# Optimization experiments

Measured on AMD Instinct MI355X. Metric: run time of the kernel, lower is better.

Reference implementation:

```python
import jax, jax.numpy as jnp
import numpy as np

B, T, C = 2, 2048, 2048
H, G, HS = 16, 4, 128       # n_head, n_query_groups, head_size
N_ELEM = 128                # rotary_percentage * head_size
D_FF = 4 * C
EPS = 1e-5


def layer_norm(x, w, b):
    mu = jnp.mean(x, axis=-1, keepdims=True)
    var = jnp.var(x, axis=-1, keepdims=True)
    return (x - mu) * jax.lax.rsqrt(var + EPS) * w + b


def apply_rope(x, cos, sin):
    # x: (B, H, T, n_elem); cos/sin: (T, n_elem) with freqs duplicated over halves
    half = x.shape[-1] // 2
    x1, x2 = x[..., :half], x[..., half:]
    rotated = jnp.concatenate((-x2, x1), axis=-1)
    return x * cos + rotated * sin


def setup_inputs() -> dict:
    key = jax.random.key(0)
    ks = jax.random.split(key, 8)
    x = jax.random.normal(ks[0], (B, T, C), dtype=jnp.float32)
    # RoPE cache (neox/llama style, duplicated halves to match half-rotation apply_rope)
    inv_freq = 1.0 / (10000.0 ** (jnp.arange(0, N_ELEM, 2, dtype=jnp.float32) / N_ELEM))
    freqs = jnp.outer(jnp.arange(T, dtype=jnp.float32), inv_freq)  # (T, n_elem/2)
    cos = jnp.concatenate((jnp.cos(freqs), jnp.cos(freqs)), axis=-1)
    sin = jnp.concatenate((jnp.sin(freqs), jnp.sin(freqs)), axis=-1)
    mask = jnp.tril(jnp.ones((T, T), dtype=bool))
    s = 0.02
    qkv_w = jax.random.normal(ks[1], ((H + 2 * G) * HS, C), dtype=jnp.float32) * s
    proj_w = jax.random.normal(ks[2], (C, C), dtype=jnp.float32) * s
    fc1_w = jax.random.normal(ks[3], (D_FF, C), dtype=jnp.float32) * s
    fc2_w = jax.random.normal(ks[4], (C, D_FF), dtype=jnp.float32) * s
    return {
        "x": x, "cos": cos, "sin": sin, "mask": mask,
        "ln1_w": jnp.ones((C,), jnp.float32), "ln1_b": jnp.zeros((C,), jnp.float32),
        "qkv_w": qkv_w, "proj_w": proj_w,
        "ln2_w": jnp.ones((C,), jnp.float32), "ln2_b": jnp.zeros((C,), jnp.float32),
        "fc1_w": fc1_w, "fc1_b": jnp.zeros((D_FF,), jnp.float32),
        "fc2_w": fc2_w, "fc2_b": jnp.zeros((C,), jnp.float32),
    }


def block_forward(x, cos, sin, mask, ln1_w, ln1_b, qkv_w, proj_w,
                  ln2_w, ln2_b, fc1_w, fc1_b, fc2_w, fc2_b):
    q_per_kv = H // G
    # --- LayerNormLinear: LN then fused QKV projection ---
    qkv = layer_norm(x, ln1_w, ln1_b) @ qkv_w.T            # (B, T, (H+2G)*HS)
    qkv = qkv.reshape(B, T, G, q_per_kv + 2, HS).transpose(0, 2, 3, 1, 4)
    q = qkv[:, :, :q_per_kv]                               # (B, G, q_per_kv, T, HS)
    k = qkv[:, :, q_per_kv:q_per_kv + 1]                   # (B, G, 1, T, HS)
    v = qkv[:, :, q_per_kv + 1:]
    # GQA expansion (repeat_interleave over the per-group axis)
    k = jnp.repeat(k, q_per_kv, axis=2)
    v = jnp.repeat(v, q_per_kv, axis=2)
    q = q.reshape(B, H, T, HS)
    k = k.reshape(B, H, T, HS)
    v = v.reshape(B, H, T, HS)
    # --- RoPE on first N_ELEM channels ---
    q = jnp.concatenate((apply_rope(q[..., :N_ELEM], cos, sin), q[..., N_ELEM:]), axis=-1)
    k = jnp.concatenate((apply_rope(k[..., :N_ELEM], cos, sin), k[..., N_ELEM:]), axis=-1)
    # --- SDPA with boolean mask ---
    scale = 1.0 / jnp.sqrt(jnp.asarray(HS, q.dtype))
    att = jnp.einsum("bhqd,bhkd->bhqk", q, k) * scale
    att = jnp.where(mask, att, jnp.finfo(att.dtype).min)
    att = jax.nn.softmax(att, axis=-1)
    y = jnp.einsum("bhqk,bhkd->bhqd", att, v)
    y = y.transpose(0, 2, 1, 3).reshape(B, T, C)
    h = y @ proj_w.T
    # --- non-parallel residual: x += attn; x += MLP(LN(x)) ---
    x = x + h
    mlp = jax.nn.gelu(layer_norm(x, ln2_w, ln2_b) @ fc1_w.T + fc1_b, approximate=False)
    x = x + (mlp @ fc2_w.T + fc2_b)
    return x


def reference(x, cos, sin, mask, ln1_w, ln1_b, qkv_w, proj_w,
              ln2_w, ln2_b, fc1_w, fc1_b, fc2_w, fc2_b):
    return block_forward(x, cos, sin, mask, ln1_w, ln1_b, qkv_w, proj_w,
                         ln2_w, ln2_b, fc1_w, fc1_b, fc2_w, fc2_b)
```

## Files before the change

### kernel.cpp

```cpp
#include <hip/hip_runtime.h>

typedef __bf16 bf16;
typedef __bf16 bf16x8 __attribute__((ext_vector_type(8)));
typedef __bf16 bf16x4 __attribute__((ext_vector_type(4)));
typedef float  f32x4  __attribute__((ext_vector_type(4)));

#define LOG2E 1.4426950408889634f

__device__ __forceinline__ void gload_lds16(const void* g, void* l) {
    __builtin_amdgcn_global_load_lds(
        (__attribute__((address_space(1))) const void*)g,
        (__attribute__((address_space(3))) void*)l, 16, 0, 0);
}

__global__ __launch_bounds__(256) void cvt_bf16(const float* __restrict__ src,
                                                bf16* __restrict__ dst, int n) {
    int i = (blockIdx.x * 256 + threadIdx.x) * 4;
    if (i + 3 < n) {
        float4 v = *(const float4*)(src + i);
        bf16x4 o;
        o[0] = (bf16)v.x; o[1] = (bf16)v.y; o[2] = (bf16)v.z; o[3] = (bf16)v.w;
        *(bf16x4*)(dst + i) = o;
    }
}

__global__ __launch_bounds__(256) void ln_kernel(const float* __restrict__ x,
                                                 const float* __restrict__ wgt,
                                                 const float* __restrict__ bias,
                                                 bf16* __restrict__ out) {
    __shared__ float red[8];
    const int tid = threadIdx.x;
    const int lane = tid & 63, w = tid >> 6;
    const size_t row = blockIdx.x;
    const float4* xr = (const float4*)(x + row * 2048);
    float4 v0 = xr[tid];
    float4 v1 = xr[tid + 256];
    float s = v0.x + v0.y + v0.z + v0.w + v1.x + v1.y + v1.z + v1.w;
    float q = v0.x*v0.x + v0.y*v0.y + v0.z*v0.z + v0.w*v0.w
            + v1.x*v1.x + v1.y*v1.y + v1.z*v1.z + v1.w*v1.w;
    #pragma unroll
    for (int off = 32; off; off >>= 1) {
        s += __shfl_xor(s, off);
        q += __shfl_xor(q, off);
    }
    if (lane == 0) { red[w] = s; red[4 + w] = q; }
    __syncthreads();
    float S  = red[0] + red[1] + red[2] + red[3];
    float Q2 = red[4] + red[5] + red[6] + red[7];
    float mu = S * (1.0f / 2048.0f);
    float var = Q2 * (1.0f / 2048.0f) - mu * mu;
    float rstd = rsqrtf(var + 1e-5f);

    bf16* orow = out + row * 2048;
    int c0 = tid * 4;
    float vv[8] = {v0.x, v0.y, v0.z, v0.w, v1.x, v1.y, v1.z, v1.w};
    bf16x4 o;
    #pragma unroll
    for (int k = 0; k < 4; ++k)
        o[k] = (bf16)((vv[k] - mu) * rstd * wgt[c0 + k] + bias[c0 + k]);
    *(bf16x4*)(orow + c0) = o;
    #pragma unroll
    for (int k = 0; k < 4; ++k)
        o[k] = (bf16)((vv[4 + k] - mu) * rstd * wgt[1024 + c0 + k] + bias[1024 + c0 + k]);
    *(bf16x4*)(orow + 1024 + c0) = o;
}

template <int EPI>
__global__ __launch_bounds__(512, 4) void gemmB(const bf16* __restrict__ A,
                                                const bf16* __restrict__ B,
                                                void* __restrict__ OutP,
                                                const float* __restrict__ bias,
                                                const float* __restrict__ res,
                                                int M, int N, int K) {
    __shared__ __align__(16) char lds[65536];
    const int tid = threadIdx.x;
    const int lane = tid & 63;
    const int w = tid >> 6, wr = w >> 1, wc = w & 1;
    const int lo = lane & 15, hi = lane >> 4;

    const int nwg = gridDim.x;
    const int bid = blockIdx.x;
    const int q = nwg >> 3, r = nwg & 7, xcd = bid & 7, off = bid >> 3;
    const int s = (xcd < r ? xcd * (q + 1) : r * (q + 1) + (xcd - r) * q) + off;
    const int MB = M / 128;
    const int sq = s >> 6, wi = s & 63;
    const int nsqm = MB >> 3;
    const int gm = sq % nsqm, gn = sq / nsqm;
    const int brow = (gm * 8 + (wi & 7)) * 128;
    const int bcol = (gn * 8 + (wi >> 3)) * 128;

    const int sr = tid >> 3;
    const int su = (tid & 7) ^ (sr & 7);
    const bf16* Ag = A + (size_t)(brow + sr) * K + su * 8;
    const bf16* Bg = B + (size_t)(bcol + sr) * K + su * 8;
    const size_t K64 = (size_t)64 * K;
    char* dst0 = lds + tid * 16;

    auto stage = [&](int bf, int kt) {
        char* d = dst0 + bf * 32768;
        gload_lds16(Ag + kt * 64, d);
        gload_lds16(Ag + K64 + kt * 64, d + 8192);
        gload_lds16(Bg + kt * 64, d + 16384);
        gload_lds16(Bg + K64 + kt * 64, d + 24576);
    };

    f32x4 acc[2][4] = {};
    const int NT = K >> 6;

    stage(0, 0);
    for (int kt = 0; kt < NT; ++kt) {
        const int cur = kt & 1;
        if (kt + 1 < NT) {
            stage(cur ^ 1, kt + 1);
            asm volatile("s_waitcnt vmcnt(4)" ::: "memory");
        } else {
            asm volatile("s_waitcnt vmcnt(0)" ::: "memory");
        }
        __builtin_amdgcn_s_barrier();

        const char* ab = lds + cur * 32768;
        const char* bb = ab + 16384;
        bf16x8 af[2][2], bfv[4][2];
        #pragma unroll
        for (int m = 0; m < 2; ++m) {
            const int rA = wr * 32 + m * 16 + lo;
            #pragma unroll
            for (int ks = 0; ks < 2; ++ks)
                af[m][ks] = *(const bf16x8*)(ab + rA * 128 + (((ks * 4 + hi) ^ (lo & 7)) << 4));
        }
        #pragma unroll
        for (int n = 0; n < 4; ++n) {
            const int rB = wc * 64 + n * 16 + lo;
            #pragma unroll
            for (int ks = 0; ks < 2; ++ks)
                bfv[n][ks] = *(const bf16x8*)(bb + rB * 128 + (((ks * 4 + hi) ^ (lo & 7)) << 4));
        }
        __builtin_amdgcn_s_setprio(1);
        #pragma unroll
        for (int m = 0; m < 2; ++m)
            #pragma unroll
            for (int n = 0; n < 4; ++n)
                #pragma unroll
                for (int ks = 0; ks < 2; ++ks)
                    acc[m][n] = __builtin_amdgcn_mfma_f32_16x16x32_bf16(af[m][ks], bfv[n][ks], acc[m][n], 0, 0, 0);
        __builtin_amdgcn_s_setprio(0);
        __builtin_amdgcn_s_barrier();
    }

    float* outF = (float*)OutP;
    bf16*  outB = (bf16*)OutP;
    #pragma unroll
    for (int n = 0; n < 4; ++n) {
        const int col = bcol + wc * 64 + n * 16 + lo;
        float bv = 0.f;
        if (EPI == 1 || EPI == 3) bv = bias[col];
        #pragma unroll
        for (int m = 0; m < 2; ++m) {
            #pragma unroll
            for (int rr = 0; rr < 4; ++rr) {
                const int row = brow + wr * 32 + m * 16 + hi * 4 + rr;
                float v = acc[m][n][rr];
                if (EPI == 0) {
                    outB[(size_t)row * N + col] = (bf16)v;
                } else if (EPI == 1) {
                    v += bv;
                    v = 0.5f * v * (1.0f + erff(v * 0.70710678118654752f));
                    outB[(size_t)row * N + col] = (bf16)v;
                } else if (EPI == 2) {
                    outF[(size_t)row * N + col] = res[(size_t)row * N + col] + v;
                } else {
                    outF[(size_t)row * N + col] = res[(size_t)row * N + col] + v + bv;
                }
            }
        }
    }
}

__global__ __launch_bounds__(256) void rope_scatter(const bf16* __restrict__ qkv,
                                                    const float* __restrict__ cosb,
                                                    const float* __restrict__ sinb,
                                                    bf16* __restrict__ Q,
                                                    bf16* __restrict__ Kg) {
    const int tid = threadIdx.x;
    const int row = blockIdx.x;
    const int b = row >> 11, t = row & 2047;
    const bf16* src = qkv + (size_t)row * 3072;
    #pragma unroll
    for (int i = tid; i < 1280; i += 256) {
        int slot = i >> 6;
        int d = i & 63;
        int g = slot / 5, m = slot - g * 5;
        int msrc = g * 6 + m;
        float v1 = (float)src[msrc * 128 + d];
        float v2 = (float)src[msrc * 128 + d + 64];
        float c1 = cosb[t * 128 + d],      s1 = sinb[t * 128 + d];
        float c2 = cosb[t * 128 + d + 64], s2 = sinb[t * 128 + d + 64];
        float o1 = v1 * c1 - v2 * s1;
        float o2 = v2 * c2 + v1 * s2;
        if (m < 4) {
            int hh = g * 4 + m;
            size_t base = ((size_t)(b * 16 + hh) * 2048 + t) * 128;
            Q[base + d] = (bf16)o1;
            Q[base + d + 64] = (bf16)o2;
        } else {
            size_t base = ((size_t)(b * 4 + g) * 2048 + t) * 128;
            Kg[base + d] = (bf16)o1;
            Kg[base + d + 64] = (bf16)o2;
        }
    }
}

__global__ __launch_bounds__(256) void vtrans(const bf16* __restrict__ qkvo,
                                              bf16* __restrict__ Vt) {
    const int tid = threadIdx.x;
    const int t0 = blockIdx.x * 64;
    const int z  = blockIdx.y;
    const int b = z >> 2, g = z & 3;
    const int d = tid & 127;
    const int th = tid >> 7;
    const bf16* src = qkvo + (size_t)(b * 2048 + t0 + th * 32) * 3072 + g * 768 + 640 + d;
    bf16* dst = Vt + ((size_t)z * 128 + d) * 2048 + t0 + th * 32;
    #pragma unroll
    for (int c = 0; c < 4; ++c) {
        bf16x8 v;
        #pragma unroll
        for (int j = 0; j < 8; ++j)
            v[j] = src[(size_t)(c * 8 + j) * 3072];
        *(bf16x8*)(dst + c * 8) = v;
    }
}

__global__ __launch_bounds__(256) void attn_kernel(const bf16* __restrict__ Q,
                                                   const bf16* __restrict__ Kg,
                                                   const bf16* __restrict__ Vt,
                                                   bf16* __restrict__ Y) {
    __shared__ __align__(16) bf16 Ks[2][64 * 128];
    __shared__ __align__(16) bf16 Vs[2][128 * 64];
    __shared__ __align__(16) bf16 Ps[4][16 * 80];

    const int tid = threadIdx.x;
    const int lane = tid & 63, w = tid >> 6;
    const int lo = lane & 15, hi = lane >> 4;
    const int bh = blockIdx.y;
    const int b = bh >> 4, h = bh & 15;
    const int g = h >> 2;

    const bf16* Kbase = Kg + (size_t)(b * 4 + g) * 2048 * 128;
    const bf16* Vbase = Vt + (size_t)(b * 4 + g) * 128 * 2048;
    const float scale = 0.08838834764831845f;
    bf16* pw = &Ps[w][0];

    bf16x8 kreg[4], vreg[4];

    #pragma unroll 1
    for (int pass = 0; pass < 2; ++pass) {
        const int qt = pass ? 31 - (int)blockIdx.x : (int)blockIdx.x;
        const int q0 = qt * 64;

        bf16x8 qf[4];
        {
            const size_t qbase = ((size_t)bh * 2048 + q0 + w * 16 + lo) * 128;
            #pragma unroll
            for (int dd = 0; dd < 4; ++dd)
                qf[dd] = *(const bf16x8*)(Q + qbase + dd * 32 + hi * 8);
        }

        float m_r[4], l_r[4];
        f32x4 oacc[8] = {};
        #pragma unroll
        for (int rr = 0; rr < 4; ++rr) { m_r[rr] = -1e30f; l_r[rr] = 0.f; }

        #pragma unroll
        for (int it = 0; it < 4; ++it) {
            int ob = (it * 256 + tid) * 16;
            int rk = ob >> 8, cb = ob & 255;
            kreg[it] = *(const bf16x8*)(Kbase + (size_t)rk * 128 + (cb >> 1));
            int dv = ob >> 7, cv = ob & 127;
            vreg[it] = *(const bf16x8*)(Vbase + (size_t)dv * 2048 + (cv >> 1));
        }
        #pragma unroll
        for (int it = 0; it < 4; ++it) {
            int ob = (it * 256 + tid) * 16;
            int rk = ob >> 8, cb = ob & 255;
            *(bf16x8*)((char*)Ks[0] + rk * 256 + (cb ^ ((rk & 7) << 4))) = kreg[it];
            int dv = ob >> 7, cv = ob & 127;
            *(bf16x8*)((char*)Vs[0] + dv * 128 + (cv ^ ((dv & 7) << 4))) = vreg[it];
        }
        __syncthreads();
        int cur = 0;

        for (int kt = 0; kt <= qt; ++kt) {
            const bool pf = (kt < qt);
            if (pf) {
                #pragma unroll
                for (int it = 0; it < 4; ++it) {
                    int ob = (it * 256 + tid) * 16;
                    int rk = ob >> 8, cb = ob & 255;
                    kreg[it] = *(const bf16x8*)(Kbase + (size_t)((kt + 1) * 64 + rk) * 128 + (cb >> 1));
                    int dv = ob >> 7, cv = ob & 127;
                    vreg[it] = *(const bf16x8*)(Vbase + (size_t)dv * 2048 + (kt + 1) * 64 + (cv >> 1));
                }
            }

            const char* KsC = (const char*)Ks[cur];
            const char* VsC = (const char*)Vs[cur];

            f32x4 sj[4];
            __builtin_amdgcn_s_setprio(1);
            #pragma unroll
            for (int j = 0; j < 4; ++j) {
                f32x4 a = {};
                int rk = j * 16 + lo;
                #pragma unroll
                for (int dd = 0; dd < 4; ++dd) {
                    int cb = dd * 64 + hi * 16;
                    bf16x8 kf = *(const bf16x8*)(KsC + rk * 256 + (cb ^ ((rk & 7) << 4)));
                    a = __builtin_amdgcn_mfma_f32_16x16x32_bf16(qf[dd], kf, a, 0, 0, 0);
                }
                sj[j] = a;
            }
            __builtin_amdgcn_s_setprio(0);

            float sv[4][4];
            const bool diag = (kt == qt);
            #pragma unroll
            for (int j = 0; j < 4; ++j)
                #pragma unroll
                for (int rr = 0; rr < 4; ++rr) {
                    float v = sj[j][rr] * scale;
                    if (diag) {
                        int tg = kt * 64 + j * 16 + lo;
                        int qg = q0 + w * 16 + hi * 4 + rr;
                        if (tg > qg) v = -1e30f;
                    }
                    sv[j][rr] = v;
                }

            float mx[4];
            #pragma unroll
            for (int rr = 0; rr < 4; ++rr) {
                float m0 = fmaxf(fmaxf(sv[0][rr], sv[1][rr]), fmaxf(sv[2][rr], sv[3][rr]));
                #pragma unroll
                for (int off = 8; off; off >>= 1) m0 = fmaxf(m0, __shfl_xor(m0, off, 16));
                mx[rr] = m0;
            }

            bool need = false;
            #pragma unroll
            for (int rr = 0; rr < 4; ++rr) need = need || (mx[rr] > m_r[rr] + 8.0f);
            if (__any(need)) {
                #pragma unroll
                for (int rr = 0; rr < 4; ++rr) {
                    float mnew = fmaxf(m_r[rr], mx[rr]);
                    float al = exp2f((m_r[rr] - mnew) * LOG2E);
                    l_r[rr] *= al;
                    m_r[rr] = mnew;
                    #pragma unroll
                    for (int dn = 0; dn < 8; ++dn) oacc[dn][rr] *= al;
                }
            }

            float p[4][4];
            #pragma unroll
            for (int rr = 0; rr < 4; ++rr) {
                #pragma unroll
                for (int j = 0; j < 4; ++j)
                    p[j][rr] = exp2f((sv[j][rr] - m_r[rr]) * LOG2E);
                float s0 = p[0][rr] + p[1][rr] + p[2][rr] + p[3][rr];
                #pragma unroll
                for (int off = 8; off; off >>= 1) s0 += __shfl_xor(s0, off, 16);
                l_r[rr] += s0;
            }

            #pragma unroll
            for (int j = 0; j < 4; ++j)
                #pragma unroll
                for (int rr = 0; rr < 4; ++rr)
                    pw[(hi * 4 + rr) * 80 + j * 16 + lo] = (bf16)p[j][rr];

            __builtin_amdgcn_s_setprio(1);
            #pragma unroll
            for (int tc = 0; tc < 2; ++tc) {
                bf16x8 pf2 = *(const bf16x8*)(pw + lo * 80 + tc * 32 + hi * 8);
                #pragma unroll
                for (int dn = 0; dn < 8; ++dn) {
                    int rv = dn * 16 + lo;
                    int cv = tc * 64 + hi * 16;
                    bf16x8 vf = *(const bf16x8*)(VsC + rv * 128 + (cv ^ ((rv & 7) << 4)));
                    oacc[dn] = __builtin_amdgcn_mfma_f32_16x16x32_bf16(pf2, vf, oacc[dn], 0, 0, 0);
                }
            }
            __builtin_amdgcn_s_setprio(0);

            if (pf) {
                #pragma unroll
                for (int it = 0; it < 4; ++it) {
                    int ob = (it * 256 + tid) * 16;
                    int rk = ob >> 8, cb = ob & 255;
                    *(bf16x8*)((char*)Ks[cur ^ 1] + rk * 256 + (cb ^ ((rk & 7) << 4))) = kreg[it];
                    int dv = ob >> 7, cv = ob & 127;
                    *(bf16x8*)((char*)Vs[cur ^ 1] + dv * 128 + (cv ^ ((dv & 7) << 4))) = vreg[it];
                }
            }
            __syncthreads();
            cur ^= 1;
        }

        #pragma unroll
        for (int dn = 0; dn < 8; ++dn)
            #pragma unroll
            for (int rr = 0; rr < 4; ++rr) {
                int qg = q0 + w * 16 + hi * 4 + rr;
                Y[((size_t)b * 2048 + qg) * 2048 + h * 128 + dn * 16 + lo] =
                    (bf16)(oacc[dn][rr] / l_r[rr]);
            }
    }
}

extern "C" void kernel_launch(void* const* d_in, const int* in_sizes, int n_in,
                              void* d_out, int out_size, void* d_ws, size_t ws_size,
                              hipStream_t stream) {
    const float* x      = (const float*)d_in[0];
    const float* cosb   = (const float*)d_in[1];
    const float* sinb   = (const float*)d_in[2];
    const float* ln1_w  = (const float*)d_in[4];
    const float* ln1_b  = (const float*)d_in[5];
    const float* qkv_w  = (const float*)d_in[6];
    const float* proj_w = (const float*)d_in[7];
    const float* ln2_w  = (const float*)d_in[8];
    const float* ln2_b  = (const float*)d_in[9];
    const float* fc1_w  = (const float*)d_in[10];
    const float* fc1_b  = (const float*)d_in[11];
    const float* fc2_w  = (const float*)d_in[12];
    const float* fc2_b  = (const float*)d_in[13];
    float* out = (float*)d_out;

    char* ws = (char*)d_ws;
    bf16*  w_qkv  = (bf16*)(ws + 0ull);
    bf16*  w_proj = (bf16*)(ws + 12582912ull);
    bf16*  w_fc1  = (bf16*)(ws + 20971520ull);
    bf16*  w_fc2  = (bf16*)(ws + 54525952ull);
    float* x2     = (float*)(ws + 88080384ull);
    bf16*  lnout  = (bf16*)(ws + 121634816ull);
    char*  R      = ws + 138412032ull;
    bf16*  qkvo = (bf16*)(R);
    bf16*  Qb   = (bf16*)(R + 25165824ull);
    bf16*  Kb   = (bf16*)(R + 41943040ull);
    bf16*  Vtb  = (bf16*)(R + 46137344ull);
    bf16*  Yb   = (bf16*)(R + 50331648ull);
    bf16*  mlp  = (bf16*)(R);

    cvt_bf16<<<6144,  256, 0, stream>>>(qkv_w,  w_qkv,  3072 * 2048);
    cvt_bf16<<<4096,  256, 0, stream>>>(proj_w, w_proj, 2048 * 2048);
    cvt_bf16<<<16384, 256, 0, stream>>>(fc1_w,  w_fc1,  8192 * 2048);
    cvt_bf16<<<16384, 256, 0, stream>>>(fc2_w,  w_fc2,  2048 * 8192);

    ln_kernel<<<4096, 256, 0, stream>>>(x, ln1_w, ln1_b, lnout);

    gemmB<0><<<768, 512, 0, stream>>>(lnout, w_qkv, qkvo, nullptr, nullptr,
                                      4096, 3072, 2048);

    rope_scatter<<<4096, 256, 0, stream>>>(qkvo, cosb, sinb, Qb, Kb);
    vtrans<<<dim3(32, 8), 256, 0, stream>>>(qkvo, Vtb);

    attn_kernel<<<dim3(16, 32), 256, 0, stream>>>(Qb, Kb, Vtb, Yb);

    gemmB<2><<<512, 512, 0, stream>>>(Yb, w_proj, x2, nullptr, x,
                                      4096, 2048, 2048);

    ln_kernel<<<4096, 256, 0, stream>>>(x2, ln2_w, ln2_b, lnout);

    gemmB<1><<<2048, 512, 0, stream>>>(lnout, w_fc1, mlp, fc1_b, nullptr,
                                       4096, 8192, 2048);

    gemmB<3><<<512, 512, 0, stream>>>(mlp, w_fc2, out, fc2_b, x2,
                                      4096, 2048, 8192);
}
```

Before: 584.1 us.

## Use 256x256-tile GEMM with XCD-aware swizzle and split-K for MLP

Adds a new GEMM kernel with 256x256 output tiles per 512-thread block, double-buffered direct-to-LDS loads, XCD-aware block remapping with super-tile grouping, and setprio around MFMA bursts. It is used for fc1 (with fused GELU) and for fc2, which is split into two K halves. One half writes the residual-plus-bias result and the other writes a float partial, summed afterwards by an extra add kernel. The larger tiles aim to raise operand reuse and L2 locality, while split-K keeps enough blocks for fc2. The cost is an extra fp32 partial buffer round-trip and higher register pressure.

```diff
diff --git a/kernel.cpp b/kernel.cpp
--- a/kernel.cpp
+++ b/kernel.cpp
@@ -21,6 +21,17 @@
         bf16x4 o;
         o[0] = (bf16)v.x; o[1] = (bf16)v.y; o[2] = (bf16)v.z; o[3] = (bf16)v.w;
         *(bf16x4*)(dst + i) = o;
+    }
+}
+
+__global__ __launch_bounds__(256) void add_f32(float* __restrict__ out,
+                                               const float* __restrict__ p, int n) {
+    int i = (blockIdx.x * 256 + threadIdx.x) * 4;
+    if (i + 3 < n) {
+        float4 a = *(const float4*)(out + i);
+        float4 b = *(const float4*)(p + i);
+        a.x += b.x; a.y += b.y; a.z += b.z; a.w += b.w;
+        *(float4*)(out + i) = a;
     }
 }
 
@@ -170,6 +181,121 @@
                     outF[(size_t)row * N + col] = res[(size_t)row * N + col] + v;
                 } else {
                     outF[(size_t)row * N + col] = res[(size_t)row * N + col] + v + bv;
+                }
+            }
+        }
+    }
+}
+
+template <int EPI>
+__global__ __launch_bounds__(512, 2) void gemmE2(const bf16* __restrict__ A,
+                                                 const bf16* __restrict__ B,
+                                                 void* __restrict__ OutP,
+                                                 const float* __restrict__ bias,
+                                                 const float* __restrict__ res,
+                                                 float* __restrict__ Aux,
+                                                 int M, int N, int Kc, int ldk,
+                                                 int SQR, int SQC) {
+    extern __shared__ __align__(16) char lds[];
+    const int tid = threadIdx.x;
+    const int lane = tid & 63;
+    const int w = tid >> 6, wr = w >> 2, wc = w & 3;
+    const int lo = lane & 15, hi = lane >> 4;
+    const int koff = (EPI == 5) ? (int)blockIdx.y * Kc : 0;
+
+    const int nwg = gridDim.x;
+    const int bid = blockIdx.x;
+    const int q = nwg >> 3, r = nwg & 7, xcd = bid & 7, off = bid >> 3;
+    const int s = (xcd < r ? xcd * (q + 1) : r * (q + 1) + (xcd - r) * q) + off;
+    const int MB = M / 256;
+    const int sqsz = SQR * SQC;
+    const int sq = s / sqsz, wi = s % sqsz;
+    const int nsqm = MB / SQR;
+    const int gm = sq % nsqm, gn = sq / nsqm;
+    const int brow = (gm * SQR + wi % SQR) * 256;
+    const int bcol = (gn * SQC + wi / SQR) * 256;
+
+    const int srow = tid >> 2;
+    const int scol = ((tid & 3) ^ ((tid >> 3) & 3)) * 8;
+    const bf16* Ag = A + (size_t)(brow + srow) * ldk + koff + scol;
+    const bf16* Bg = B + (size_t)(bcol + srow) * ldk + koff + scol;
+    const size_t R128 = (size_t)128 * ldk;
+    char* d0 = lds + tid * 16;
+
+    auto stage = [&](int bf, int kt) {
+        char* d = d0 + bf * 32768;
+        gload_lds16(Ag + kt * 32, d);
+        gload_lds16(Ag + R128 + kt * 32, d + 8192);
+        gload_lds16(Bg + kt * 32, d + 16384);
+        gload_lds16(Bg + R128 + kt * 32, d + 24576);
+    };
+
+    f32x4 acc[8][4] = {};
+    const int NT = Kc >> 5;
+    const int xsl = (hi ^ ((lo >> 1) & 3)) << 4;
+
+    stage(0, 0);
+    #pragma unroll 1
+    for (int kt = 0; kt < NT; ++kt) {
+        const int cur = kt & 1;
+        if (kt + 1 < NT) {
+            stage(cur ^ 1, kt + 1);
+            asm volatile("s_waitcnt vmcnt(4)" ::: "memory");
+        } else {
+            asm volatile("s_waitcnt vmcnt(0)" ::: "memory");
+        }
+        __builtin_amdgcn_s_barrier();
+
+        const char* ab = lds + cur * 32768;
+        const char* bb = ab + 16384;
+        bf16x8 af[8], bv[4];
+        #pragma unroll
+        for (int m = 0; m < 4; ++m)
+            af[m] = *(const bf16x8*)(ab + (wr * 128 + m * 16 + lo) * 64 + xsl);
+        #pragma unroll
+        for (int n = 0; n < 4; ++n)
+            bv[n] = *(const bf16x8*)(bb + (wc * 64 + n * 16 + lo) * 64 + xsl);
+        __builtin_amdgcn_s_setprio(1);
+        #pragma unroll
+        for (int m = 0; m < 4; ++m)
+            #pragma unroll
+            for (int n = 0; n < 4; ++n)
+                acc[m][n] = __builtin_amdgcn_mfma_f32_16x16x32_bf16(af[m], bv[n], acc[m][n], 0, 0, 0);
+        __builtin_amdgcn_s_setprio(0);
+        #pragma unroll
+        for (int m = 4; m < 8; ++m)
+            af[m] = *(const bf16x8*)(ab + (wr * 128 + m * 16 + lo) * 64 + xsl);
+        __builtin_amdgcn_s_setprio(1);
+        #pragma unroll
+        for (int m = 4; m < 8; ++m)
+            #pragma unroll
+            for (int n = 0; n < 4; ++n)
+                acc[m][n] = __builtin_amdgcn_mfma_f32_16x16x32_bf16(af[m], bv[n], acc[m][n], 0, 0, 0);
+        __builtin_amdgcn_s_setprio(0);
+        __builtin_amdgcn_s_barrier();
+    }
+
+    float* outF = (float*)OutP;
+    bf16*  outB = (bf16*)OutP;
+    #pragma unroll
+    for (int n = 0; n < 4; ++n) {
+        const int col = bcol + wc * 64 + n * 16 + lo;
+        float bv2 = bias ? bias[col] : 0.f;
+        #pragma unroll
+        for (int m = 0; m < 8; ++m) {
+            #pragma unroll
+            for (int rr = 0; rr < 4; ++rr) {
+                const int row = brow + wr * 128 + m * 16 + hi * 4 + rr;
+                float v = acc[m][n][rr];
+                if (EPI == 1) {
+                    v += bv2;
+                    v = 0.5f * v * (1.0f + erff(v * 0.70710678118654752f));
+                    outB[(size_t)row * N + col] = (bf16)v;
+                } else if (EPI == 5) {
+                    if (blockIdx.y == 0)
+                        outF[(size_t)row * N + col] = res[(size_t)row * N + col] + v + bv2;
+                    else
+                        Aux[(size_t)row * N + col] = v;
                 }
             }
         }
@@ -449,6 +575,9 @@
     bf16*  Vtb  = (bf16*)(R + 46137344ull);
     bf16*  Yb   = (bf16*)(R + 50331648ull);
     bf16*  mlp  = (bf16*)(R);
+    float* p_fc2 = (float*)(ws + 20971520ull);
+
+    constexpr int LDSE = 65536;
 
     cvt_bf16<<<6144,  256, 0, stream>>>(qkv_w,  w_qkv,  3072 * 2048);
     cvt_bf16<<<4096,  256, 0, stream>>>(proj_w, w_proj, 2048 * 2048);
@@ -470,9 +599,10 @@
 
     ln_kernel<<<4096, 256, 0, stream>>>(x2, ln2_w, ln2_b, lnout);
 
-    gemmB<1><<<2048, 512, 0, stream>>>(lnout, w_fc1, mlp, fc1_b, nullptr,
-                                       4096, 8192, 2048);
-
-    gemmB<3><<<512, 512, 0, stream>>>(mlp, w_fc2, out, fc2_b, x2,
-                                      4096, 2048, 8192);
-}
+    gemmE2<1><<<dim3(512, 1), 512, LDSE, stream>>>(lnout, w_fc1, mlp, fc1_b, nullptr,
+                                                   nullptr, 4096, 8192, 2048, 2048, 8, 4);
+
+    gemmE2<5><<<dim3(128, 2), 512, LDSE, stream>>>(mlp, w_fc2, out, fc2_b, x2,
+                                                   p_fc2, 4096, 2048, 4096, 8192, 8, 2);
+    add_f32<<<8192, 256, 0, stream>>>(out, p_fc2, 4096 * 2048);
+}
```

New measurement: 670.0 us. +14.7%, slower.

## Add 128x128-tile 256-thread GEMM with XCD-aware swizzle for FC1

Applied to the files above, without the earlier changes.

Adds a new GEMM kernel for the FC1+GELU projection. It uses 128x128 output tiles with 4 waves each computing 64x64, double-buffered direct global-to-LDS loads with an XOR swizzle, and a block-index remap that groups tiles per XCD into 8x8 super-tiles for L2 reuse. The goal is more MFMA work per LDS load and better cache locality than the previous 512-thread kernel. It also uses more accumulator registers per thread and a K-step of only 32, which may leave the loop barrier-bound.

```diff
diff --git a/kernel.cpp b/kernel.cpp
--- a/kernel.cpp
+++ b/kernel.cpp
@@ -171,6 +171,97 @@
                 } else {
                     outF[(size_t)row * N + col] = res[(size_t)row * N + col] + v + bv;
                 }
+            }
+        }
+    }
+}
+
+template <int EPI>
+__global__ __launch_bounds__(256, 4) void gemmC2(const bf16* __restrict__ A,
+                                                 const bf16* __restrict__ B,
+                                                 void* __restrict__ OutP,
+                                                 const float* __restrict__ bias,
+                                                 int M, int N, int K) {
+    __shared__ __align__(16) char lds[32768];
+    const int tid = threadIdx.x;
+    const int lane = tid & 63;
+    const int w = tid >> 6, wr = w >> 1, wc = w & 1;
+    const int lo = lane & 15, hi = lane >> 4;
+
+    const int nwg = gridDim.x;
+    const int bid = blockIdx.x;
+    const int q = nwg >> 3, r = nwg & 7, xcd = bid & 7, off = bid >> 3;
+    const int s = (xcd < r ? xcd * (q + 1) : r * (q + 1) + (xcd - r) * q) + off;
+    const int MB = M / 128;
+    const int sq = s >> 6, wi = s & 63;
+    const int nsqm = MB >> 3;
+    const int gm = sq % nsqm, gn = sq / nsqm;
+    const int brow = (gm * 8 + (wi & 7)) * 128;
+    const int bcol = (gn * 8 + (wi >> 3)) * 128;
+
+    const int srow = tid >> 2;
+    const int scol = ((tid & 3) ^ ((tid >> 3) & 3)) * 8;
+    const bf16* Ag = A + (size_t)(brow + srow) * K + scol;
+    const bf16* Bg = B + (size_t)(bcol + srow) * K + scol;
+    const size_t R64 = (size_t)64 * K;
+    char* d0 = lds + tid * 16;
+
+    auto stage = [&](int bf, int kt) {
+        char* d = d0 + bf * 16384;
+        gload_lds16(Ag + kt * 32, d);
+        gload_lds16(Ag + R64 + kt * 32, d + 4096);
+        gload_lds16(Bg + kt * 32, d + 8192);
+        gload_lds16(Bg + R64 + kt * 32, d + 12288);
+    };
+
+    f32x4 acc[4][4] = {};
+    const int NT = K >> 5;
+    const int xsl = (hi ^ ((lo >> 1) & 3)) << 4;
+
+    stage(0, 0);
+    #pragma unroll 1
+    for (int kt = 0; kt < NT; ++kt) {
+        const int cur = kt & 1;
+        if (kt + 1 < NT) {
+            stage(cur ^ 1, kt + 1);
+            asm volatile("s_waitcnt vmcnt(4)" ::: "memory");
+        } else {
+            asm volatile("s_waitcnt vmcnt(0)" ::: "memory");
+        }
+        __builtin_amdgcn_s_barrier();
+
+        const char* ab = lds + cur * 16384;
+        const char* bb = ab + 8192;
+        bf16x8 af[4], bfv[4];
+        #pragma unroll
+        for (int m = 0; m < 4; ++m)
+            af[m] = *(const bf16x8*)(ab + (wr * 64 + m * 16 + lo) * 64 + xsl);
+        #pragma unroll
+        for (int n = 0; n < 4; ++n)
+            bfv[n] = *(const bf16x8*)(bb + (wc * 64 + n * 16 + lo) * 64 + xsl);
+        __builtin_amdgcn_s_setprio(1);
+        #pragma unroll
+        for (int m = 0; m < 4; ++m)
+            #pragma unroll
+            for (int n = 0; n < 4; ++n)
+                acc[m][n] = __builtin_amdgcn_mfma_f32_16x16x32_bf16(af[m], bfv[n], acc[m][n], 0, 0, 0);
+        __builtin_amdgcn_s_setprio(0);
+        __builtin_amdgcn_s_barrier();
+    }
+
+    bf16* outB = (bf16*)OutP;
+    #pragma unroll
+    for (int n = 0; n < 4; ++n) {
+        const int col = bcol + wc * 64 + n * 16 + lo;
+        const float bv = bias[col];
+        #pragma unroll
+        for (int m = 0; m < 4; ++m) {
+            #pragma unroll
+            for (int rr = 0; rr < 4; ++rr) {
+                const int row = brow + wr * 64 + m * 16 + hi * 4 + rr;
+                float v = acc[m][n][rr] + bv;
+                v = 0.5f * v * (1.0f + erff(v * 0.70710678118654752f));
+                outB[(size_t)row * N + col] = (bf16)v;
             }
         }
     }
@@ -470,8 +561,8 @@
 
     ln_kernel<<<4096, 256, 0, stream>>>(x2, ln2_w, ln2_b, lnout);
 
-    gemmB<1><<<2048, 512, 0, stream>>>(lnout, w_fc1, mlp, fc1_b, nullptr,
-                                       4096, 8192, 2048);
+    gemmC2<1><<<2048, 256, 0, stream>>>(lnout, w_fc1, mlp, fc1_b,
+                                        4096, 8192, 2048);
 
     gemmB<3><<<512, 512, 0, stream>>>(mlp, w_fc2, out, fc2_b, x2,
                                       4096, 2048, 8192);
```

New measurement: 608.1 us. 4.1% more time.

## Add gemmF loading A directly to registers and staging only B in LDS

Applied to the files above, without the earlier changes.

Adds a new GEMM kernel for the two MLP matmuls. It loads A fragments straight from global memory into registers and stages only B tiles through LDS with global_load_lds, using double buffering. It also requests higher occupancy through launch_bounds(512,4) and sets wave priority during the MFMA section. The aim is to cut LDS traffic and shrink the LDS footprint. The risk is that A is re-read from global by each wave column without LDS sharing, and the A loads may be uncoalesced.

```diff
diff --git a/kernel.cpp b/kernel.cpp
--- a/kernel.cpp
+++ b/kernel.cpp
@@ -168,6 +168,111 @@
                     outB[(size_t)row * N + col] = (bf16)v;
                 } else if (EPI == 2) {
                     outF[(size_t)row * N + col] = res[(size_t)row * N + col] + v;
+                } else {
+                    outF[(size_t)row * N + col] = res[(size_t)row * N + col] + v + bv;
+                }
+            }
+        }
+    }
+}
+
+template <int EPI>
+__global__ __launch_bounds__(512, 4) void gemmF(const bf16* __restrict__ A,
+                                                const bf16* __restrict__ B,
+                                                void* __restrict__ OutP,
+                                                const float* __restrict__ bias,
+                                                const float* __restrict__ res,
+                                                int M, int N, int K) {
+    __shared__ __align__(16) char lds[32768];
+    const int tid = threadIdx.x;
+    const int lane = tid & 63;
+    const int w = tid >> 6, wr = w >> 1, wc = w & 1;
+    const int lo = lane & 15, hi = lane >> 4;
+
+    const int nwg = gridDim.x;
+    const int bid = blockIdx.x;
+    const int q = nwg >> 3, r = nwg & 7, xcd = bid & 7, off = bid >> 3;
+    const int s = (xcd < r ? xcd * (q + 1) : r * (q + 1) + (xcd - r) * q) + off;
+    const int MB = M / 128;
+    const int sq = s >> 6, wi = s & 63;
+    const int nsqm = MB >> 3;
+    const int gm = sq % nsqm, gn = sq / nsqm;
+    const int brow = (gm * 8 + (wi & 7)) * 128;
+    const int bcol = (gn * 8 + (wi >> 3)) * 128;
+
+    const int sr = tid >> 3;
+    const int su = (tid & 7) ^ (sr & 7);
+    const bf16* Bg = B + (size_t)(bcol + sr) * K + su * 8;
+    const size_t K64 = (size_t)64 * K;
+    char* dst0 = lds + tid * 16;
+    auto stageB = [&](int bf, int kt) {
+        char* d = dst0 + bf * 16384;
+        gload_lds16(Bg + kt * 64, d);
+        gload_lds16(Bg + K64 + kt * 64, d + 8192);
+    };
+
+    const bf16* Aw = A + (size_t)(brow + wr * 32 + lo) * K + hi * 8;
+    const size_t AR16 = (size_t)16 * K;
+
+    bf16x8 aA[2][2], aB[2][2], bfv[4][2];
+    f32x4 acc[2][4] = {};
+    const int NT = K >> 6;
+
+#define ISSUEA(SET, KT) { _Pragma("unroll") for (int m = 0; m < 2; ++m) { \
+    _Pragma("unroll") for (int ks = 0; ks < 2; ++ks) { \
+        SET[m][ks] = *(const bf16x8*)(Aw + (size_t)m * AR16 + (KT) * 64 + ks * 32); } } }
+
+#define COMPUTEF(SET, BUF) { \
+    const char* bb = lds + (BUF) * 16384; \
+    _Pragma("unroll") for (int n = 0; n < 4; ++n) { \
+        const int rB = wc * 64 + n * 16 + lo; \
+        _Pragma("unroll") for (int ks = 0; ks < 2; ++ks) { \
+            bfv[n][ks] = *(const bf16x8*)(bb + rB * 128 + (((ks * 4 + hi) ^ (lo & 7)) << 4)); } } \
+    __builtin_amdgcn_s_setprio(1); \
+    _Pragma("unroll") for (int m = 0; m < 2; ++m) { \
+    _Pragma("unroll") for (int n = 0; n < 4; ++n) { \
+    _Pragma("unroll") for (int ks = 0; ks < 2; ++ks) { \
+        acc[m][n] = __builtin_amdgcn_mfma_f32_16x16x32_bf16(SET[m][ks], bfv[n][ks], acc[m][n], 0, 0, 0); } } } \
+    __builtin_amdgcn_s_setprio(0); }
+
+    ISSUEA(aA, 0); stageB(0, 0);
+    #pragma unroll 1
+    for (int t = 0; t < NT; t += 2) {
+        ISSUEA(aB, t + 1); stageB(1, t + 1);
+        asm volatile("s_waitcnt vmcnt(6)" ::: "memory");
+        __builtin_amdgcn_s_barrier();
+        COMPUTEF(aA, 0)
+        __builtin_amdgcn_s_barrier();
+        if (t + 2 < NT) {
+            ISSUEA(aA, t + 2); stageB(0, t + 2);
+            asm volatile("s_waitcnt vmcnt(6)" ::: "memory");
+        } else {
+            asm volatile("s_waitcnt vmcnt(0)" ::: "memory");
+        }
+        __builtin_amdgcn_s_barrier();
+        COMPUTEF(aB, 1)
+        __builtin_amdgcn_s_barrier();
+    }
+#undef ISSUEA
+#undef COMPUTEF
+
+    float* outF = (float*)OutP;
+    bf16*  outB = (bf16*)OutP;
+    #pragma unroll
+    for (int n = 0; n < 4; ++n) {
+        const int col = bcol + wc * 64 + n * 16 + lo;
+        float bv = 0.f;
+        if (EPI == 1 || EPI == 3) bv = bias[col];
+        #pragma unroll
+        for (int m = 0; m < 2; ++m) {
+            #pragma unroll
+            for (int rr = 0; rr < 4; ++rr) {
+                const int row = brow + wr * 32 + m * 16 + hi * 4 + rr;
+                float v = acc[m][n][rr];
+                if (EPI == 1) {
+                    v += bv;
+                    v = 0.5f * v * (1.0f + erff(v * 0.70710678118654752f));
+                    outB[(size_t)row * N + col] = (bf16)v;
                 } else {
                     outF[(size_t)row * N + col] = res[(size_t)row * N + col] + v + bv;
                 }
@@ -470,9 +575,9 @@
 
     ln_kernel<<<4096, 256, 0, stream>>>(x2, ln2_w, ln2_b, lnout);
 
-    gemmB<1><<<2048, 512, 0, stream>>>(lnout, w_fc1, mlp, fc1_b, nullptr,
+    gemmF<1><<<2048, 512, 0, stream>>>(lnout, w_fc1, mlp, fc1_b, nullptr,
                                        4096, 8192, 2048);
 
-    gemmB<3><<<512, 512, 0, stream>>>(mlp, w_fc2, out, fc2_b, x2,
+    gemmF<3><<<512, 512, 0, stream>>>(mlp, w_fc2, out, fc2_b, x2,
                                       4096, 2048, 8192);
 }
```

Measured after the change: 858.8 us. +47.0%, slower.
